# Optimization experiments

Hardware: AMD Instinct MI355X
Metric: run time of the kernel (lower is better)

## Reference

```python
import jax, jax.numpy as jnp
import numpy as np

B, S, D, H, DFF = 4, 2048, 1024, 16, 4096
DK = D // H
EPS = 1e-6


def layernorm(x, w, b):
    # Faithful to source: unbiased std (ddof=1), divides by (std + eps).
    mean = jnp.mean(x, axis=-1, keepdims=True)
    std = jnp.std(x, axis=-1, keepdims=True, ddof=1)
    return w * (x - mean) / (std + EPS) + b


def setup_inputs() -> dict:
    key = jax.random.key(0)
    ks = jax.random.split(key, 16)
    g = lambda k, shape: (jax.random.normal(k, shape, dtype=jnp.float32) * 0.02)
    inp = {
        "x": jax.random.normal(ks[0], (B, S, D), dtype=jnp.float32),
        "mask": jnp.ones((B, 1, 1, S), dtype=jnp.int32),
        # attention projections (stored [in, out]; math identical to torch Linear)
        "wq": g(ks[1], (D, D)), "bq": jnp.zeros((D,), jnp.float32),
        "wk": g(ks[2], (D, D)), "bk": jnp.zeros((D,), jnp.float32),
        "wv": g(ks[3], (D, D)), "bv": jnp.zeros((D,), jnp.float32),
        "wo": g(ks[4], (D, D)), "bo": jnp.zeros((D,), jnp.float32),
        # feed-forward
        "w1": g(ks[5], (D, DFF)), "b1": jnp.zeros((DFF,), jnp.float32),
        "w2": g(ks[6], (DFF, D)), "b2": jnp.zeros((D,), jnp.float32),
        # layer norms
        "ln1_w": jnp.ones((D,), jnp.float32), "ln1_b": jnp.zeros((D,), jnp.float32),
        "ln2_w": jnp.ones((D,), jnp.float32), "ln2_b": jnp.zeros((D,), jnp.float32),
    }
    return inp


def attention(xn, mask, wq, bq, wk, bk, wv, bv, wo, bo):
    q = (xn @ wq + bq).reshape(B, S, H, DK)
    k = (xn @ wk + bk).reshape(B, S, H, DK)
    v = (xn @ wv + bv).reshape(B, S, H, DK)
    scores = jnp.einsum("bqhd,bkhd->bhqk", q, k) / jnp.sqrt(jnp.float32(DK))
    scores = jnp.where(mask == 0, -jnp.inf, scores)
    attn = jax.nn.softmax(scores, axis=-1)  # dropout identity at inference
    out = jnp.einsum("bhqk,bkhd->bqhd", attn, v).reshape(B, S, D)
    return out @ wo + bo


def reference(x, mask, wq, bq, wk, bk, wv, bv, wo, bo,
              w1, b1, w2, b2, ln1_w, ln1_b, ln2_w, ln2_b):
    # pre-norm residual 1: self-attention
    x = x + attention(layernorm(x, ln1_w, ln1_b), mask,
                      wq, bq, wk, bk, wv, bv, wo, bo)
    # pre-norm residual 2: FFN
    xn = layernorm(x, ln2_w, ln2_b)
    ffn = jax.nn.relu(xn @ w1 + b1) @ w2 + b2
    return x + ffn
```

## Files before the change

### kernel.cpp

```cpp
#include <hip/hip_runtime.h>


typedef unsigned short u16;
typedef unsigned u32;
typedef __bf16 bf16x8 __attribute__((ext_vector_type(8)));
typedef float f32x4 __attribute__((ext_vector_type(4)));
typedef float f32x16 __attribute__((ext_vector_type(16)));

typedef __attribute__((address_space(1))) const void* as1_cvp;
typedef __attribute__((address_space(3))) void* as3_vp;

__device__ __forceinline__ void async_copy16(const void* g, void* l) {
  __builtin_amdgcn_global_load_lds((as1_cvp)g, (as3_vp)l, 16, 0, 0);
}

__device__ __forceinline__ u16 f2bf(float f) {
  unsigned u = __float_as_uint(f);
  u += 0x7fffu + ((u >> 16) & 1u);
  return (u16)(u >> 16);
}

__device__ __forceinline__ float fast_exp2(float x) {
  return __builtin_amdgcn_exp2f(x);
}

__device__ __forceinline__ u32 cvt_pk_bf16(float lo, float hi) {
  u32 d;
  asm("v_cvt_pk_bf16_f32 %0, %1, %2" : "=v"(d) : "v"(lo), "v"(hi));
  return d;
}

__device__ __forceinline__ void permlane32_swap(u32& x, u32& y) {
  asm volatile("v_permlane32_swap_b32 %0, %1" : "+v"(x), "+v"(y));
}

__global__ __launch_bounds__(256) void k_transpose_bf16(
    const float* __restrict__ src, u16* __restrict__ dst, int K, int N,
    float scale) {
  __shared__ float tile[32][33];
  int n0 = blockIdx.x * 32, k0 = blockIdx.y * 32;
  int c = threadIdx.x & 31, r0 = threadIdx.x >> 5;
#pragma unroll
  for (int i = 0; i < 32; i += 8)
    tile[r0 + i][c] = src[(size_t)(k0 + r0 + i) * N + n0 + c];
  __syncthreads();
#pragma unroll
  for (int i = 0; i < 32; i += 8)
    dst[(size_t)(n0 + r0 + i) * K + k0 + c] = f2bf(tile[c][r0 + i] * scale);
}

__global__ __launch_bounds__(256) void k_pack_bias(
    const float* __restrict__ bq, const float* __restrict__ bk,
    const float* __restrict__ bv, float* __restrict__ out, float qscale) {
  int i = blockIdx.x * 256 + threadIdx.x;
  float v;
  if (i < 1024) v = bq[i] * qscale;
  else if (i < 2048) v = bk[i - 1024];
  else v = bv[i - 2048];
  out[i] = v;
}

__global__ __launch_bounds__(256) void k_maskadd(
    const int* __restrict__ mask, float* __restrict__ madd) {
  int i = blockIdx.x * 256 + threadIdx.x;
  madd[i] = mask[i] ? 0.0f : -1e30f;
}

__global__ __launch_bounds__(256) void k_layernorm_bf16(
    const float* __restrict__ x, const float* __restrict__ w,
    const float* __restrict__ b, u16* __restrict__ out) {
  const int D = 1024;
  int row = blockIdx.x, tid = threadIdx.x;
  const float4* xr = (const float4*)(x + (size_t)row * D);
  float4 v = xr[tid];
  float s = v.x + v.y + v.z + v.w;
  float ss = v.x * v.x + v.y * v.y + v.z * v.z + v.w * v.w;
#pragma unroll
  for (int off = 1; off < 64; off <<= 1) {
    s += __shfl_xor(s, off);
    ss += __shfl_xor(ss, off);
  }
  __shared__ float rs[4], rss[4];
  int wave = tid >> 6, lane = tid & 63;
  if (lane == 0) { rs[wave] = s; rss[wave] = ss; }
  __syncthreads();
  float S_ = rs[0] + rs[1] + rs[2] + rs[3];
  float SS = rss[0] + rss[1] + rss[2] + rss[3];
  float mean = S_ * (1.0f / D);
  float var = (SS - (float)D * mean * mean) * (1.0f / (D - 1));
  float inv = 1.0f / (sqrtf(fmaxf(var, 0.0f)) + 1e-6f);
  float4 wv = ((const float4*)w)[tid], bv = ((const float4*)b)[tid];
  u16* orow = out + (size_t)row * D + tid * 4;
  orow[0] = f2bf(wv.x * (v.x - mean) * inv + bv.x);
  orow[1] = f2bf(wv.y * (v.y - mean) * inv + bv.y);
  orow[2] = f2bf(wv.z * (v.z - mean) * inv + bv.z);
  orow[3] = f2bf(wv.w * (v.w - mean) * inv + bv.w);
}

template <bool RELU, bool HAS_RES, bool OUT_BF16>
__global__ __launch_bounds__(256) void k_gemm(
    const u16* __restrict__ A, const u16* __restrict__ Bt,
    const float* __restrict__ bias, const float* __restrict__ res,
    void* __restrict__ outp, int M, int N, int K) {
  __shared__ __align__(16) u16 As[128 * 32];
  __shared__ __align__(16) u16 Bs[128 * 32];
  const int tid = threadIdx.x;
  const int lane = tid & 63, wave = tid >> 6;
  const int quad = lane >> 4, l16 = lane & 15;
  const int m0 = blockIdx.y * 128, n0 = blockIdx.x * 128;
  const int wm = (wave >> 1) * 64, wn = (wave & 1) * 64;

  const int r0 = tid >> 2, o0 = (tid & 3) * 8;
  const u16* a0 = A + (size_t)(m0 + r0) * K + o0;
  const u16* a1 = A + (size_t)(m0 + r0 + 64) * K + o0;
  const u16* b0p = Bt + (size_t)(n0 + r0) * K + o0;
  const u16* b1p = Bt + (size_t)(n0 + r0 + 64) * K + o0;
  u16* lA0 = As + tid * 8;  u16* lA1 = As + (tid + 256) * 8;
  u16* lB0 = Bs + tid * 8;  u16* lB1 = Bs + (tid + 256) * 8;

  f32x4 zero = {0.0f, 0.0f, 0.0f, 0.0f};
  f32x4 acc[4][4];
#pragma unroll
  for (int i = 0; i < 4; i++)
#pragma unroll
    for (int j = 0; j < 4; j++) acc[i][j] = zero;

  for (int k0 = 0; k0 < K; k0 += 32) {
    __syncthreads();
    async_copy16(a0 + k0, lA0);
    async_copy16(a1 + k0, lA1);
    async_copy16(b0p + k0, lB0);
    async_copy16(b1p + k0, lB1);
    __syncthreads();
    bf16x8 af[4], bfr[4];
#pragma unroll
    for (int mb = 0; mb < 4; mb++)
      af[mb] = *(const bf16x8*)&As[(wm + mb * 16 + l16) * 32 + quad * 8];
#pragma unroll
    for (int nb = 0; nb < 4; nb++)
      bfr[nb] = *(const bf16x8*)&Bs[(wn + nb * 16 + l16) * 32 + quad * 8];
#pragma unroll
    for (int mb = 0; mb < 4; mb++)
#pragma unroll
      for (int nb = 0; nb < 4; nb++)
        acc[mb][nb] = __builtin_amdgcn_mfma_f32_16x16x32_bf16(
            af[mb], bfr[nb], acc[mb][nb], 0, 0, 0);
  }
#pragma unroll
  for (int mb = 0; mb < 4; mb++) {
#pragma unroll
    for (int nb = 0; nb < 4; nb++) {
      int col = n0 + wn + nb * 16 + l16;
      float bb = bias[col];
#pragma unroll
      for (int r = 0; r < 4; r++) {
        int row = m0 + wm + mb * 16 + quad * 4 + r;
        float vv = acc[mb][nb][r] + bb;
        if (HAS_RES) vv += res[(size_t)row * N + col];
        if (RELU) vv = fmaxf(vv, 0.0f);
        if (OUT_BF16) ((u16*)outp)[(size_t)row * N + col] = f2bf(vv);
        else ((float*)outp)[(size_t)row * N + col] = vv;
      }
    }
  }
}

__global__ __launch_bounds__(512, 4) void k_attention(
    const u16* __restrict__ qkv, const float* __restrict__ madd,
    u16* __restrict__ out) {
  const int S = 2048, D = 1024, QS = 3072;
  int blk = blockIdx.x;
  int xcd = blk & 7, t = blk >> 3;
  int qt = t & 7, gg = t >> 3;
  int g = gg * 8 + xcd;
  int h = g & 15, bb = g >> 4;
  int tid = threadIdx.x, lane = tid & 63, wave = tid >> 6;
  int l32 = lane & 31, hh = lane >> 5;

  __shared__ __align__(16) u16 Ks[64 * 64];
  __shared__ __align__(16) u16 Vs[64 * 64];

  const int qrowbase = bb * S + qt * 256;
  const int sbase = bb * S;
  const int qrow = qrowbase + wave * 32 + l32;

  bf16x8 qf[4];
  {
    const u16* qp = qkv + (size_t)qrow * QS + h * 64 + 8 * hh;
#pragma unroll
    for (int c = 0; c < 4; c++) qf[c] = *(const bf16x8*)(qp + 16 * c);
  }

  bf16x8 ones;
  {
    union { u16 s[8]; bf16x8 v; } o_;
#pragma unroll
    for (int j = 0; j < 8; j++) o_.s[j] = 0x3F80;
    ones = o_.v;
  }

  f32x16 accA, accB, lacc;
#pragma unroll
  for (int r = 0; r < 16; r++) { accA[r] = 0.0f; accB[r] = 0.0f; lacc[r] = 0.0f; }

  const int krow = tid >> 3, ko = ((tid & 7) ^ (krow & 7)) * 8;
  const int vkey = tid >> 3, vf = tid & 7;

  for (int kt = 0; kt < 32; kt++) {
    const int kb0 = sbase + kt * 64;
    __syncthreads();
    async_copy16(qkv + (size_t)(kb0 + krow) * QS + 1024 + h * 64 + ko,
                 Ks + tid * 8);
    {
      union { uint4 u; u16 s[8]; } tt;
      tt.u = *(const uint4*)(qkv + (size_t)(kb0 + vkey) * QS + 2048 + h * 64 +
                             vf * 8);
#pragma unroll
      for (int j = 0; j < 8; j++)
        Vs[(8 * vf + j) * 64 + (vkey ^ (8 * (vf ^ j)))] = tt.s[j];
    }
    __syncthreads();

    u32 pa[4][4];
#pragma unroll
    for (int kb = 0; kb < 2; kb++) {
      const int kr = kb * 32 + l32;
      f32x16 sc;
#pragma unroll
      for (int r = 0; r < 16; r++) sc[r] = 0.0f;
#pragma unroll
      for (int c = 0; c < 4; c++) {
        bf16x8 kf = *(const bf16x8*)&Ks[kr * 64 + (((2 * c + hh) ^ (kr & 7)) * 8)];
        sc = __builtin_amdgcn_mfma_f32_32x32x16_bf16(kf, qf[c], sc, 0, 0, 0);
      }
      f32x4 mv0 = *(const f32x4*)(madd + kb0 + kb * 32 + 0 + 4 * hh);
      f32x4 mv1 = *(const f32x4*)(madd + kb0 + kb * 32 + 8 + 4 * hh);
      f32x4 mv2 = *(const f32x4*)(madd + kb0 + kb * 32 + 16 + 4 * hh);
      f32x4 mv3 = *(const f32x4*)(madd + kb0 + kb * 32 + 24 + 4 * hh);
#pragma unroll
      for (int r = 0; r < 4; r++) sc[r] = fast_exp2(sc[r] + mv0[r]);
#pragma unroll
      for (int r = 0; r < 4; r++) sc[4 + r] = fast_exp2(sc[4 + r] + mv1[r]);
#pragma unroll
      for (int r = 0; r < 4; r++) sc[8 + r] = fast_exp2(sc[8 + r] + mv2[r]);
#pragma unroll
      for (int r = 0; r < 4; r++) sc[12 + r] = fast_exp2(sc[12 + r] + mv3[r]);
#pragma unroll
      for (int hk = 0; hk < 2; hk++) {
        u32 a0 = cvt_pk_bf16(sc[hk * 8 + 0], sc[hk * 8 + 1]);
        u32 a1 = cvt_pk_bf16(sc[hk * 8 + 2], sc[hk * 8 + 3]);
        u32 b0 = cvt_pk_bf16(sc[hk * 8 + 4], sc[hk * 8 + 5]);
        u32 b1 = cvt_pk_bf16(sc[hk * 8 + 6], sc[hk * 8 + 7]);
        permlane32_swap(a0, b0);
        permlane32_swap(a1, b1);
        pa[kb * 2 + hk][0] = a0;
        pa[kb * 2 + hk][1] = a1;
        pa[kb * 2 + hk][2] = b0;
        pa[kb * 2 + hk][3] = b1;
      }
    }
#pragma unroll
    for (int kc = 0; kc < 4; kc++) {
      union { u32 u[4]; bf16x8 v; } pu;
      pu.u[0] = pa[kc][0]; pu.u[1] = pa[kc][1];
      pu.u[2] = pa[kc][2]; pu.u[3] = pa[kc][3];
      lacc = __builtin_amdgcn_mfma_f32_32x32x16_bf16(pu.v, ones, lacc, 0, 0, 0);
      const int kch = 2 * kc + hh;
      const int r0v = l32;
      bf16x8 v0 =
          *(const bf16x8*)&Vs[r0v * 64 + ((kch ^ (((r0v >> 3) ^ r0v) & 7)) * 8)];
      accA = __builtin_amdgcn_mfma_f32_32x32x16_bf16(pu.v, v0, accA, 0, 0, 0);
      const int r1v = 32 + l32;
      bf16x8 v1 =
          *(const bf16x8*)&Vs[r1v * 64 + ((kch ^ (((r1v >> 3) ^ r1v) & 7)) * 8)];
      accB = __builtin_amdgcn_mfma_f32_32x32x16_bf16(pu.v, v1, accB, 0, 0, 0);
    }
  }
#pragma unroll
  for (int r = 0; r < 16; r++) {
    float inv = 1.0f / lacc[r];
    size_t row = (size_t)(qrowbase + wave * 32 + (r & 3) + 8 * (r >> 2) + 4 * hh);
    u16* op = out + row * D + h * 64;
    op[l32] = f2bf(accA[r] * inv);
    op[32 + l32] = f2bf(accB[r] * inv);
  }
}

extern "C" void kernel_launch(void* const* d_in, const int* in_sizes, int n_in,
                              void* d_out, int out_size, void* d_ws,
                              size_t ws_size, hipStream_t stream) {
  const float* x    = (const float*)d_in[0];
  const int*   mask = (const int*)d_in[1];
  const float* wq = (const float*)d_in[2];   const float* bq = (const float*)d_in[3];
  const float* wk = (const float*)d_in[4];   const float* bk = (const float*)d_in[5];
  const float* wv = (const float*)d_in[6];   const float* bv = (const float*)d_in[7];
  const float* wo = (const float*)d_in[8];   const float* bo = (const float*)d_in[9];
  const float* w1 = (const float*)d_in[10];  const float* b1 = (const float*)d_in[11];
  const float* w2 = (const float*)d_in[12];  const float* b2 = (const float*)d_in[13];
  const float* ln1w = (const float*)d_in[14]; const float* ln1b = (const float*)d_in[15];
  const float* ln2w = (const float*)d_in[16]; const float* ln2b = (const float*)d_in[17];
  float* outp = (float*)d_out;

  char* ws = (char*)d_ws;
  const size_t MB = 1024 * 1024;
  u16* wqkvT = (u16*)(ws + 0 * MB);
  u16* woT   = (u16*)(ws + 6 * MB);
  u16* w1T   = (u16*)(ws + 8 * MB);
  u16* w2T   = (u16*)(ws + 16 * MB);
  u16* xn    = (u16*)(ws + 24 * MB);
  u16* qkvb  = (u16*)(ws + 40 * MB);
  u16* hb    = (u16*)(ws + 40 * MB);
  float* bqkv = (float*)(ws + 88 * MB);
  float* madd = (float*)(ws + 88 * MB + 64 * 1024);
  float* y1  = (float*)(ws + 104 * MB);

  const float qscale = 0.125f * 1.44269504f;

  k_transpose_bf16<<<dim3(32, 32), 256, 0, stream>>>(wq, wqkvT, 1024, 1024, qscale);
  k_transpose_bf16<<<dim3(32, 32), 256, 0, stream>>>(wk, wqkvT + 1024 * 1024, 1024, 1024, 1.0f);
  k_transpose_bf16<<<dim3(32, 32), 256, 0, stream>>>(wv, wqkvT + 2048 * 1024, 1024, 1024, 1.0f);
  k_transpose_bf16<<<dim3(32, 32), 256, 0, stream>>>(wo, woT, 1024, 1024, 1.0f);
  k_transpose_bf16<<<dim3(128, 32), 256, 0, stream>>>(w1, w1T, 1024, 4096, 1.0f);
  k_transpose_bf16<<<dim3(32, 128), 256, 0, stream>>>(w2, w2T, 4096, 1024, 1.0f);
  k_pack_bias<<<12, 256, 0, stream>>>(bq, bk, bv, bqkv, qscale);
  k_maskadd<<<32, 256, 0, stream>>>(mask, madd);

  k_layernorm_bf16<<<8192, 256, 0, stream>>>(x, ln1w, ln1b, xn);

  k_gemm<false, false, true><<<dim3(24, 64), 256, 0, stream>>>(
      xn, wqkvT, bqkv, nullptr, qkvb, 8192, 3072, 1024);

  k_attention<<<512, 512, 0, stream>>>(qkvb, madd, xn);

  dim3 g1(8, 64);
  k_gemm<false, true, false><<<g1, 256, 0, stream>>>(xn, woT, bo, x, y1, 8192, 1024, 1024);

  k_layernorm_bf16<<<8192, 256, 0, stream>>>(y1, ln2w, ln2b, xn);

  k_gemm<true, false, true><<<dim3(32, 64), 256, 0, stream>>>(
      xn, w1T, b1, nullptr, hb, 8192, 4096, 1024);

  k_gemm<false, true, false><<<g1, 256, 0, stream>>>(hb, w2T, b2, y1, outp, 8192, 1024, 4096);
}
```

Before: 591.8 us.

## Rewrite GEMM with 256x128 tiles, triple-buffered async LDS pipeline and XOR swizzle

Replaces the single-buffered 128x128 GEMM (two barriers per 32-wide k step) with a 512-thread kernel using 256x128 tiles, BK=64, and a three-stage LDS ring fed by async global-to-LDS copies. A vmcnt wait lets loads for k-tiles t+1 and t+2 stay in flight while tile t is computed. The LDS layout is XOR-swizzled to avoid bank conflicts on fragment reads. The grid is also reordered so blockIdx.x walks M. The cost is 144KB of LDS per block and higher register pressure under launch_bounds(512,2), which may limit occupancy.

```diff
diff --git a/kernel.cpp b/kernel.cpp
--- a/kernel.cpp
+++ b/kernel.cpp
@@ -98,25 +98,36 @@
 }
 
 template <bool RELU, bool HAS_RES, bool OUT_BF16>
-__global__ __launch_bounds__(256) void k_gemm(
+__global__ __launch_bounds__(512, 2) void k_gemm2(
     const u16* __restrict__ A, const u16* __restrict__ Bt,
     const float* __restrict__ bias, const float* __restrict__ res,
     void* __restrict__ outp, int M, int N, int K) {
-  __shared__ __align__(16) u16 As[128 * 32];
-  __shared__ __align__(16) u16 Bs[128 * 32];
+  __shared__ __align__(16) u16 lds[3 * 24576];
   const int tid = threadIdx.x;
   const int lane = tid & 63, wave = tid >> 6;
   const int quad = lane >> 4, l16 = lane & 15;
-  const int m0 = blockIdx.y * 128, n0 = blockIdx.x * 128;
+  const int m0 = blockIdx.x * 256, n0 = blockIdx.y * 128;
   const int wm = (wave >> 1) * 64, wn = (wave & 1) * 64;
 
-  const int r0 = tid >> 2, o0 = (tid & 3) * 8;
-  const u16* a0 = A + (size_t)(m0 + r0) * K + o0;
-  const u16* a1 = A + (size_t)(m0 + r0 + 64) * K + o0;
-  const u16* b0p = Bt + (size_t)(n0 + r0) * K + o0;
-  const u16* b1p = Bt + (size_t)(n0 + r0 + 64) * K + o0;
-  u16* lA0 = As + tid * 8;  u16* lA1 = As + (tid + 256) * 8;
-  u16* lB0 = Bs + tid * 8;  u16* lB1 = Bs + (tid + 256) * 8;
+  const int srow = tid >> 3;
+  const int schunk8 = ((tid & 7) ^ (srow & 7)) * 8;
+  const u16* gA0 = A + (size_t)(m0 + srow) * K + schunk8;
+  const u16* gA1 = A + (size_t)(m0 + 64 + srow) * K + schunk8;
+  const u16* gA2 = A + (size_t)(m0 + 128 + srow) * K + schunk8;
+  const u16* gA3 = A + (size_t)(m0 + 192 + srow) * K + schunk8;
+  const u16* gB0 = Bt + (size_t)(n0 + srow) * K + schunk8;
+  const u16* gB1 = Bt + (size_t)(n0 + 64 + srow) * K + schunk8;
+
+  auto STAGE = [&](int t, int s) {
+    const size_t ko = (size_t)t * 64;
+    u16* sb = lds + s * 24576;
+    async_copy16(gA0 + ko, sb + tid * 8);
+    async_copy16(gA1 + ko, sb + 4096 + tid * 8);
+    async_copy16(gA2 + ko, sb + 8192 + tid * 8);
+    async_copy16(gA3 + ko, sb + 12288 + tid * 8);
+    async_copy16(gB0 + ko, sb + 16384 + tid * 8);
+    async_copy16(gB1 + ko, sb + 20480 + tid * 8);
+  };
 
   f32x4 zero = {0.0f, 0.0f, 0.0f, 0.0f};
   f32x4 acc[4][4];
@@ -125,26 +136,36 @@
 #pragma unroll
     for (int j = 0; j < 4; j++) acc[i][j] = zero;
 
-  for (int k0 = 0; k0 < K; k0 += 32) {
-    __syncthreads();
-    async_copy16(a0 + k0, lA0);
-    async_copy16(a1 + k0, lA1);
-    async_copy16(b0p + k0, lB0);
-    async_copy16(b1p + k0, lB1);
-    __syncthreads();
-    bf16x8 af[4], bfr[4];
-#pragma unroll
-    for (int mb = 0; mb < 4; mb++)
-      af[mb] = *(const bf16x8*)&As[(wm + mb * 16 + l16) * 32 + quad * 8];
-#pragma unroll
-    for (int nb = 0; nb < 4; nb++)
-      bfr[nb] = *(const bf16x8*)&Bs[(wn + nb * 16 + l16) * 32 + quad * 8];
-#pragma unroll
-    for (int mb = 0; mb < 4; mb++)
-#pragma unroll
-      for (int nb = 0; nb < 4; nb++)
-        acc[mb][nb] = __builtin_amdgcn_mfma_f32_16x16x32_bf16(
-            af[mb], bfr[nb], acc[mb][nb], 0, 0, 0);
+  STAGE(0, 0);
+  STAGE(1, 1);
+  const int NT = K >> 6;
+  for (int t = 0; t < NT; t++) {
+    asm volatile("s_waitcnt vmcnt(6)" ::: "memory");
+    __builtin_amdgcn_s_barrier();
+    if (t + 2 < NT) STAGE(t + 2, (t + 2) % 3);
+    const u16* sb = lds + (t % 3) * 24576;
+    const u16* sbB = sb + 16384;
+#pragma unroll
+    for (int ks = 0; ks < 2; ks++) {
+      bf16x8 af[4], bfr[4];
+#pragma unroll
+      for (int mb = 0; mb < 4; mb++) {
+        int R = wm + mb * 16 + l16;
+        af[mb] = *(const bf16x8*)&sb[R * 64 + (((4 * ks + quad) ^ (R & 7)) * 8)];
+      }
+#pragma unroll
+      for (int nb = 0; nb < 4; nb++) {
+        int C = wn + nb * 16 + l16;
+        bfr[nb] =
+            *(const bf16x8*)&sbB[C * 64 + (((4 * ks + quad) ^ (C & 7)) * 8)];
+      }
+#pragma unroll
+      for (int mb = 0; mb < 4; mb++)
+#pragma unroll
+        for (int nb = 0; nb < 4; nb++)
+          acc[mb][nb] = __builtin_amdgcn_mfma_f32_16x16x32_bf16(
+              af[mb], bfr[nb], acc[mb][nb], 0, 0, 0);
+    }
   }
 #pragma unroll
   for (int mb = 0; mb < 4; mb++) {
@@ -327,18 +348,18 @@
 
   k_layernorm_bf16<<<8192, 256, 0, stream>>>(x, ln1w, ln1b, xn);
 
-  k_gemm<false, false, true><<<dim3(24, 64), 256, 0, stream>>>(
+  k_gemm2<false, false, true><<<dim3(32, 24), 512, 0, stream>>>(
       xn, wqkvT, bqkv, nullptr, qkvb, 8192, 3072, 1024);
 
   k_attention<<<512, 512, 0, stream>>>(qkvb, madd, xn);
 
-  dim3 g1(8, 64);
-  k_gemm<false, true, false><<<g1, 256, 0, stream>>>(xn, woT, bo, x, y1, 8192, 1024, 1024);
+  dim3 go(32, 8);
+  k_gemm2<false, true, false><<<go, 512, 0, stream>>>(xn, woT, bo, x, y1, 8192, 1024, 1024);
 
   k_layernorm_bf16<<<8192, 256, 0, stream>>>(y1, ln2w, ln2b, xn);
 
-  k_gemm<true, false, true><<<dim3(32, 64), 256, 0, stream>>>(
+  k_gemm2<true, false, true><<<dim3(32, 32), 512, 0, stream>>>(
       xn, w1T, b1, nullptr, hb, 8192, 4096, 1024);
 
-  k_gemm<false, true, false><<<g1, 256, 0, stream>>>(hb, w2T, b2, y1, outp, 8192, 1024, 4096);
-}
+  k_gemm2<false, true, false><<<go, 512, 0, stream>>>(hb, w2T, b2, y1, outp, 8192, 1024, 4096);
+}
```

Result: faster. 500.6 us (-15.4%).
